# Kernel optimization log

Hardware: AMD Instinct MI355X
Metric: run time of the kernel (lower is better)

The kernel has to match this reference:

```python
import jax, jax.numpy as jnp
import numpy as np
from jax import lax

L1_PENALTY = 0.01
ALPHA = L1_PENALTY / (2.0 * 1024.0)  # matches self.l1_penalty = l1_penalty / (2*1024)
N_ITERS = 200      # fixed FISTA iteration budget (replaces sklearn CD to tol=1e-6)
POWER_ITERS = 30   # power iterations for Lipschitz constant


def setup_inputs() -> dict:
    key = jax.random.key(0)
    k1, k2 = jax.random.split(key)
    D = jax.random.normal(k1, (10000, 1024), dtype=jnp.float32)
    D = D / (jnp.linalg.norm(D, axis=1, keepdims=True) + 1e-12)  # unit-norm concept embeddings
    emb = jax.random.normal(k2, (128, 1024), dtype=jnp.float32)
    emb = emb / (jnp.linalg.norm(emb, axis=1, keepdims=True) + 1e-12)  # unit-norm CLIP embeddings
    return {"embedding": emb, "dictionary": D}


def _lipschitz(D):
    # Largest eigenvalue of (1/n) * X^T X where X = D.T (n = clip_dim = n_samples in sklearn's Lasso objective)
    n = jnp.asarray(D.shape[1], D.dtype)
    v = jnp.ones((D.shape[0],), D.dtype)

    def body(i, v):
        u = v @ D                 # [d]
        v = (u @ D.T) / n         # [K]
        return v / (jnp.linalg.norm(v) + 1e-12)

    v = lax.fori_loop(0, POWER_ITERS, body, v)
    u = v @ D
    return jnp.linalg.norm((u @ D.T) / n)


def _nn_lasso_fista(D, Y):
    # Batched nonnegative Lasso: min_w (1/(2n))||y - D^T w||^2 + alpha*||w||_1, w >= 0
    # Same objective sklearn.linear_model.Lasso(alpha, positive=True, fit_intercept=False) solves per sample.
    n = jnp.asarray(D.shape[1], D.dtype)
    L = _lipschitz(D)
    step = 1.0 / L
    thresh = step * jnp.asarray(ALPHA, D.dtype)
    B, K = Y.shape[0], D.shape[0]
    w0 = jnp.zeros((B, K), Y.dtype)

    def body(i, carry):
        w, z, t = carry
        grad = ((z @ D - Y) @ D.T) / n                 # [B,K] gradient of smooth part
        w_new = jnp.maximum(z - step * grad - thresh, 0.0)  # nonnegative soft-threshold prox
        t_new = 0.5 * (1.0 + jnp.sqrt(1.0 + 4.0 * t * t))
        z_new = w_new + ((t - 1.0) / t_new) * (w_new - w)
        return (w_new, z_new, t_new)

    w, _, _ = lax.fori_loop(0, N_ITERS, body, (w0, w0, jnp.asarray(1.0, Y.dtype)))
    return w


def reference(embedding, dictionary):
    # decompose: per-sample nonnegative Lasso weights, batched
    weights = _nn_lasso_fista(dictionary, embedding)          # [B, K]
    # recompose_vector: weights @ dictionary, then L2-normalize rows
    recon = weights @ dictionary                              # [B, d]
    recon = recon / (jnp.linalg.norm(recon, axis=1, keepdims=True) + 1e-12)
    # encode_vector: diag(recon @ embedding.T).sum() == sum_i <recon_i, emb_i>
    score = jnp.sum(recon * embedding)
    return (weights, score)
```

## Files before the change

### kernel.cpp

```cpp
#include <hip/hip_runtime.h>
#include <math.h>

#define N_ITERS 200
#define PRECISE_TAIL 16
#define FAST_ITERS (N_ITERS - PRECISE_TAIL)
#define B_DIM 128
#define K_DIM 10000
#define KP2 10240
#define KB  10048
#define D_DIM 1024
#define ALPHA_F 4.8828125e-6f
#define SPLITK 32
#define KSLICE 320
#define NSTEP1 10
#define LSCALE 2048.0f
#define INV_LSCALE 4.8828125e-4f

typedef unsigned short u16;
typedef __attribute__((ext_vector_type(8))) _Float16 f16x8;
typedef __attribute__((ext_vector_type(4))) float f32x4;
#define MFMA16 __builtin_amdgcn_mfma_f32_16x16x32_f16

__device__ __forceinline__ u16 f2h(float x) {
    _Float16 h = (_Float16)x;
    return __builtin_bit_cast(unsigned short, h);
}
__device__ __forceinline__ float h2f(u16 v) {
    _Float16 h = __builtin_bit_cast(_Float16, v);
    return (float)h;
}
__device__ __forceinline__ void split2h(float x, u16& h, u16& l) {
    u16 hh = f2h(x);
    h = hh;
    l = f2h((x - h2f(hh)) * LSCALE);
}
__device__ __forceinline__ int swz(int r) { return (r & 3) ^ ((r >> 2) & 1); }

__device__ __forceinline__ void gl2lds16(const u16* g, u16* l) {
    __builtin_amdgcn_global_load_lds(
        (const __attribute__((address_space(1))) unsigned int*)g,
        (__attribute__((address_space(3))) unsigned int*)l,
        16, 0, 0);
}

template<int TN, int KS, bool SP>
__device__ __forceinline__ void gcore(
        const u16* __restrict__ Ahg, const u16* __restrict__ Alg, size_t sA, int arow0,
        const u16* __restrict__ Bhg, const u16* __restrict__ Blg, size_t sB, int brow0,
        size_t k0, int nsteps, u16* lds, int t, f32x4 (*acc)[2]) {
    constexpr int MFRAG = (TN == 64) ? 4 : 2;
    constexpr int P = KS / 32;
    constexpr int NA = P * (SP ? 2 : 1);
    constexpr int AB0 = NA * 4096;
    constexpr int BPAN = TN * 32;
    constexpr int NBP = P * (SP ? 2 : 1);
    constexpr int BUFS = AB0 + NBP * BPAN;
    constexpr int LA = 2 * NA;
    constexpr int LB = (TN == 64) ? (SP ? 2 : 1) : 1;
    constexpr int NLD = LA + LB;
    int lane = t & 63, quad = lane >> 4, lr = lane & 15;
    int wv = t >> 6;
    int wm = (TN == 64) ? ((wv >> 1) * 64) : (wv * 32);
    int wn = (TN == 64) ? ((wv & 1) * 32) : 0;
    int r1 = t >> 2, qs = t & 3;
    int q1 = qs ^ swz(r1);
    const u16* pA[NA][2];
    #pragma unroll
    for (int pa = 0; pa < NA; ++pa) {
        const u16* base = (!SP || pa < P) ? Ahg : Alg;
        size_t kk = k0 + (size_t)(pa % P) * 32;
        pA[pa][0] = base + (size_t)(arow0 + r1) * sA + kk + q1 * 8;
        pA[pa][1] = base + (size_t)(arow0 + r1 + 64) * sA + kk + q1 * 8;
    }
    const u16* pB0;
    const u16* pB1 = nullptr;
    int bdst;
    if constexpr (TN == 64) {
        pB0 = Bhg + (size_t)(brow0 + r1) * sB + k0 + q1 * 8;
        if constexpr (SP) pB1 = Blg + (size_t)(brow0 + r1) * sB + k0 + q1 * 8;
        bdst = AB0 + t * 8;
    } else {
        int j = t >> 7;
        int rb = (t & 127) >> 2;
        int qb = qs ^ swz(rb);
        if constexpr (SP) {
            pB0 = (j ? Blg : Bhg) + (size_t)(brow0 + rb) * sB + k0 + qb * 8;
        } else {
            pB0 = Bhg + (size_t)(brow0 + rb) * sB + k0 + (size_t)j * 32 + qb * 8;
        }
        bdst = AB0 + j * BPAN + (t & 127) * 8;
    }
    int dA = t * 8;
    int offA[MFRAG], offB[2];
    #pragma unroll
    for (int mi = 0; mi < MFRAG; ++mi) { int rr = wm + mi * 16 + lr; offA[mi] = rr * 32 + ((quad ^ swz(rr)) * 8); }
    #pragma unroll
    for (int ni = 0; ni < 2; ++ni) { int rr = wn + ni * 16 + lr; offB[ni] = rr * 32 + ((quad ^ swz(rr)) * 8); }
    f32x4 accC[MFRAG][2];
    #pragma unroll
    for (int mi = 0; mi < MFRAG; ++mi)
        #pragma unroll
        for (int ni = 0; ni < 2; ++ni) { acc[mi][ni] = (f32x4){0.f,0.f,0.f,0.f}; accC[mi][ni] = (f32x4){0.f,0.f,0.f,0.f}; }

    auto stage = [&](u16* b, int c) {
        #pragma unroll
        for (int pa = 0; pa < NA; ++pa) {
            gl2lds16(pA[pa][0] + c, b + pa * 4096 + dA);
            gl2lds16(pA[pa][1] + c, b + pa * 4096 + 2048 + dA);
        }
        gl2lds16(pB0 + c, b + bdst);
        if constexpr (TN == 64 && SP) gl2lds16(pB1 + c, b + bdst + BPAN);
    };
    stage(lds, 0);
    if (nsteps > 1) stage(lds + BUFS, KS);

    for (int s = 0; s < nsteps; ++s) {
        if (s + 2 < nsteps) stage(lds + ((s + 2) % 3) * BUFS, (s + 2) * KS);
        if (s + 3 <= nsteps) {
            asm volatile("s_waitcnt vmcnt(%0)" : : "i"(2 * NLD) : "memory");
        } else if (s + 2 == nsteps) {
            asm volatile("s_waitcnt vmcnt(%0)" : : "i"(NLD) : "memory");
        } else {
            asm volatile("s_waitcnt vmcnt(0)" : : : "memory");
        }
        __builtin_amdgcn_s_barrier();
        u16* b = lds + (s % 3) * BUFS;
        #pragma unroll
        for (int p = 0; p < P; ++p) {
            f16x8 aH[MFRAG], bH[2];
            #pragma unroll
            for (int mi = 0; mi < MFRAG; ++mi) aH[mi] = *(const f16x8*)&b[p * 4096 + offA[mi]];
            #pragma unroll
            for (int ni = 0; ni < 2; ++ni) bH[ni] = *(const f16x8*)&b[AB0 + p * BPAN + offB[ni]];
            if constexpr (SP) {
                f16x8 aL[MFRAG], bL[2];
                #pragma unroll
                for (int mi = 0; mi < MFRAG; ++mi) aL[mi] = *(const f16x8*)&b[(P + p) * 4096 + offA[mi]];
                #pragma unroll
                for (int ni = 0; ni < 2; ++ni) bL[ni] = *(const f16x8*)&b[AB0 + (P + p) * BPAN + offB[ni]];
                #pragma unroll
                for (int mi = 0; mi < MFRAG; ++mi)
                    #pragma unroll
                    for (int ni = 0; ni < 2; ++ni) {
                        acc[mi][ni]  = MFMA16(aH[mi], bH[ni], acc[mi][ni], 0, 0, 0);
                        accC[mi][ni] = MFMA16(aL[mi], bH[ni], accC[mi][ni], 0, 0, 0);
                        accC[mi][ni] = MFMA16(aH[mi], bL[ni], accC[mi][ni], 0, 0, 0);
                    }
            } else {
                #pragma unroll
                for (int mi = 0; mi < MFRAG; ++mi)
                    #pragma unroll
                    for (int ni = 0; ni < 2; ++ni)
                        acc[mi][ni] = MFMA16(aH[mi], bH[ni], acc[mi][ni], 0, 0, 0);
            }
        }
        __builtin_amdgcn_s_barrier();
    }
    if constexpr (SP) {
        #pragma unroll
        for (int mi = 0; mi < MFRAG; ++mi)
            #pragma unroll
            for (int ni = 0; ni < 2; ++ni)
                #pragma unroll
                for (int r = 0; r < 4; ++r)
                    acc[mi][ni][r] += accC[mi][ni][r] * INV_LSCALE;
    }
}

__global__ __launch_bounds__(256) void k_init(float* __restrict__ out,
                                              u16* __restrict__ Zh, u16* __restrict__ Zl,
                                              u16* __restrict__ Wh,
                                              float* __restrict__ u0,
                                              float* __restrict__ scal) {
    int idx = blockIdx.x * 256 + threadIdx.x;
    int stride = gridDim.x * 256;
    for (int i = idx; i <= B_DIM * K_DIM; i += stride) out[i] = 0.0f;
    unsigned* zh = (unsigned*)Zh;
    unsigned* zl = (unsigned*)Zl;
    for (int i = idx; i < B_DIM * KP2 / 2; i += stride) { zh[i] = 0u; zl[i] = 0u; }
    unsigned* wh = (unsigned*)Wh;
    for (int i = idx; i < B_DIM * KB / 2; i += stride) wh[i] = 0u;
    for (int i = idx; i < 64; i += stride) scal[i] = 0.0f;
    for (int i = idx; i < D_DIM; i += stride) u0[i] = 0.0f;
}

__global__ __launch_bounds__(256) void k_convertD(const float* __restrict__ D,
                                                  u16* __restrict__ Dh,
                                                  u16* __restrict__ Dl,
                                                  u16* __restrict__ Dth,
                                                  u16* __restrict__ Dtl) {
    __shared__ u16 Th[32][33], Tl[32][33];
    int tx = threadIdx.x & 31, ty = threadIdx.x >> 5;
    int k0 = blockIdx.x * 32, d0 = blockIdx.y * 32;
    #pragma unroll
    for (int r = 0; r < 4; ++r) {
        int krow = k0 + ty + r * 8;
        float val = (krow < K_DIM) ? D[(size_t)krow * D_DIM + d0 + tx] : 0.0f;
        u16 h, l; split2h(val, h, l);
        if (krow < KB) {
            Dh[(size_t)krow * D_DIM + d0 + tx] = h;
            Dl[(size_t)krow * D_DIM + d0 + tx] = l;
        }
        Th[ty + r * 8][tx] = h;
        Tl[ty + r * 8][tx] = l;
    }
    __syncthreads();
    #pragma unroll
    for (int r = 0; r < 4; ++r) {
        int d = d0 + ty + r * 8;
        int k = k0 + tx;
        Dth[(size_t)d * KP2 + k] = Th[tx][ty + r * 8];
        Dtl[(size_t)d * KP2 + k] = Tl[tx][ty + r * 8];
    }
}

__global__ __launch_bounds__(256) void k_colsum(const float* __restrict__ D,
                                                float* __restrict__ u0) {
    int t = threadIdx.x;
    int kbase = blockIdx.x * 40;
    float a0 = 0.f, a1 = 0.f, a2 = 0.f, a3 = 0.f;
    for (int k = kbase; k < kbase + 40; ++k) {
        const float* row = D + (size_t)k * D_DIM;
        a0 += row[t];
        a1 += row[t + 256];
        a2 += row[t + 512];
        a3 += row[t + 768];
    }
    atomicAdd(&u0[t], a0);
    atomicAdd(&u0[t + 256], a1);
    atomicAdd(&u0[t + 512], a2);
    atomicAdd(&u0[t + 768], a3);
}

__global__ __launch_bounds__(256, 2) void k_gram(const u16* __restrict__ Dth,
                                                 const u16* __restrict__ Dtl,
                                                 float* __restrict__ G) {
    __shared__ __align__(16) u16 lds[3 * 12288];
    int t = threadIdx.x;
    int n0 = blockIdx.x * 64, m0 = blockIdx.y * 128;
    f32x4 acc[4][2];
    gcore<64, 32, true>(Dth, Dtl, KP2, m0, Dth, Dtl, KP2, n0, 0, 320, lds, t, acc);
    int lane = t & 63, quad = lane >> 4, lr = lane & 15;
    int wv = t >> 6;
    int wm = (wv >> 1) * 64, wn = (wv & 1) * 32;
    #pragma unroll
    for (int mi = 0; mi < 4; ++mi)
        #pragma unroll
        for (int ni = 0; ni < 2; ++ni) {
            int c = n0 + wn + ni * 16 + lr;
            #pragma unroll
            for (int r = 0; r < 4; ++r) {
                int row = m0 + wm + mi * 16 + quad * 4 + r;
                G[(size_t)row * D_DIM + c] = acc[mi][ni][r];
            }
        }
}

__global__ __launch_bounds__(256) void k_pstep(const float* __restrict__ G,
                                               const float* __restrict__ u0,
                                               const float* __restrict__ wvin,
                                               float* __restrict__ wvout,
                                               float* __restrict__ scal, int pw) {
    int t = threadIdx.x;
    int c = blockIdx.x * 4 + (t >> 6);
    int lane = t & 63;
    float rsX = (pw > 0) ? rsqrtf(scal[1 + pw]) : 1.0f;
    float a = 0.f;
    const float* Gr = G + (size_t)c * D_DIM;
    #pragma unroll
    for (int j = 0; j < 16; ++j) {
        int r = lane + j * 64;
        float ur = (pw == 0) ? u0[r] : wvin[r] * rsX;
        a = fmaf(ur, Gr[r], a);
    }
    #pragma unroll
    for (int o = 32; o > 0; o >>= 1) a += __shfl_down(a, o, 64);
    if (lane == 0) {
        float uc = (pw == 0) ? u0[c] : wvin[c] * rsX;
        wvout[c] = a;
        atomicAdd(&scal[2 + pw], a * uc);
    }
}

__global__ void k_Lfin(float* __restrict__ scal) {
    float stepv = 1024.0f / sqrtf(scal[2 + 30]);
    scal[0] = stepv;
    scal[1] = stepv * ALPHA_F;
}

__global__ __launch_bounds__(256, 2) void k_g1f(const u16* __restrict__ Zh,
                                                const u16* __restrict__ Dth,
                                                float* __restrict__ Up) {
    __shared__ __align__(16) u16 lds[3 * 6144];
    int t = threadIdx.x;
    int n0 = blockIdx.x * 64;
    int ks = blockIdx.y;
    f32x4 acc[4][2];
    gcore<64, 32, false>(Zh, nullptr, KP2, 0, Dth, nullptr, KP2, n0,
                         (size_t)ks * KSLICE, NSTEP1, lds, t, acc);
    int lane = t & 63, quad = lane >> 4, lr = lane & 15;
    int wv = t >> 6;
    int wm = (wv >> 1) * 64, wn = (wv & 1) * 32;
    float* o = Up + (size_t)ks * (B_DIM * D_DIM);
    #pragma unroll
    for (int mi = 0; mi < 4; ++mi)
        #pragma unroll
        for (int ni = 0; ni < 2; ++ni) {
            int d = n0 + wn + ni * 16 + lr;
            #pragma unroll
            for (int r = 0; r < 4; ++r) {
                int row = wm + mi * 16 + quad * 4 + r;
                o[(size_t)row * D_DIM + d] = acc[mi][ni][r];
            }
        }
}

__global__ __launch_bounds__(256, 2) void k_g1p(const u16* __restrict__ Zh,
                                                const u16* __restrict__ Zl,
                                                const u16* __restrict__ Dth,
                                                const u16* __restrict__ Dtl,
                                                float* __restrict__ Up) {
    __shared__ __align__(16) u16 lds[3 * 12288];
    int t = threadIdx.x;
    int n0 = blockIdx.x * 64;
    int ks = blockIdx.y;
    f32x4 acc[4][2];
    gcore<64, 32, true>(Zh, Zl, KP2, 0, Dth, Dtl, KP2, n0, (size_t)ks * KSLICE,
                        NSTEP1, lds, t, acc);
    int lane = t & 63, quad = lane >> 4, lr = lane & 15;
    int wv = t >> 6;
    int wm = (wv >> 1) * 64, wn = (wv & 1) * 32;
    float* o = Up + (size_t)ks * (B_DIM * D_DIM);
    #pragma unroll
    for (int mi = 0; mi < 4; ++mi)
        #pragma unroll
        for (int ni = 0; ni < 2; ++ni) {
            int d = n0 + wn + ni * 16 + lr;
            #pragma unroll
            for (int r = 0; r < 4; ++r) {
                int row = wm + mi * 16 + quad * 4 + r;
                o[(size_t)row * D_DIM + d] = acc[mi][ni][r];
            }
        }
}

__global__ __launch_bounds__(256) void k_redF(const float* __restrict__ Up,
                                              u16* __restrict__ Eh,
                                              const float* __restrict__ emb) {
    int base = (blockIdx.x * 256 + threadIdx.x) * 8;
    float4 s0 = {0, 0, 0, 0}, s1 = {0, 0, 0, 0};
    #pragma unroll
    for (int s = 0; s < SPLITK; ++s) {
        const float* p = Up + (size_t)s * (B_DIM * D_DIM) + base;
        float4 a = *(const float4*)p;
        float4 b = *(const float4*)(p + 4);
        s0.x += a.x; s0.y += a.y; s0.z += a.z; s0.w += a.w;
        s1.x += b.x; s1.y += b.y; s1.z += b.z; s1.w += b.w;
    }
    float4 e0 = *(const float4*)&emb[base];
    float4 e1 = *(const float4*)&emb[base + 4];
    float vbuf[8] = {s0.x - e0.x, s0.y - e0.y, s0.z - e0.z, s0.w - e0.w,
                     s1.x - e1.x, s1.y - e1.y, s1.z - e1.z, s1.w - e1.w};
    union { u16 us[8]; int4 v; } h;
    #pragma unroll
    for (int q = 0; q < 8; ++q) h.us[q] = f2h(vbuf[q]);
    *(int4*)&Eh[base] = h.v;
}

__global__ __launch_bounds__(256) void k_redP(const float* __restrict__ Up,
                                              u16* __restrict__ Eh,
                                              u16* __restrict__ El,
                                              const float* __restrict__ emb,
                                              int recon) {
    int base = (blockIdx.x * 256 + threadIdx.x) * 8;
    float4 s0 = {0, 0, 0, 0}, s1 = {0, 0, 0, 0};
    #pragma unroll
    for (int s = 0; s < SPLITK; ++s) {
        const float* p = Up + (size_t)s * (B_DIM * D_DIM) + base;
        float4 a = *(const float4*)p;
        float4 b = *(const float4*)(p + 4);
        s0.x += a.x; s0.y += a.y; s0.z += a.z; s0.w += a.w;
        s1.x += b.x; s1.y += b.y; s1.z += b.z; s1.w += b.w;
    }
    if (!recon) {
        float4 e0 = *(const float4*)&emb[base];
        float4 e1 = *(const float4*)&emb[base + 4];
        s0.x -= e0.x; s0.y -= e0.y; s0.z -= e0.z; s0.w -= e0.w;
        s1.x -= e1.x; s1.y -= e1.y; s1.z -= e1.z; s1.w -= e1.w;
    }
    float vbuf[8] = {s0.x, s0.y, s0.z, s0.w, s1.x, s1.y, s1.z, s1.w};
    union { u16 us[8]; int4 v; } h, l;
    #pragma unroll
    for (int q = 0; q < 8; ++q) split2h(vbuf[q], h.us[q], l.us[q]);
    *(int4*)&Eh[base] = h.v;
    *(int4*)&El[base] = l.v;
}

template<int EM>
__global__ __launch_bounds__(256, 2) void k_g2f(const u16* __restrict__ Eh,
                                                const u16* __restrict__ Dh,
                                                u16* __restrict__ Wh,
                                                float* __restrict__ W,
                                                u16* __restrict__ Zh,
                                                u16* __restrict__ Zl,
                                                const float* __restrict__ scal,
                                                float mom) {
    __shared__ __align__(16) u16 lds[3 * 10240];
    int t = threadIdx.x;
    int n0 = blockIdx.x * 32;
    f32x4 acc[2][2];
    gcore<32, 64, false>(Eh, nullptr, D_DIM, 0, Dh, nullptr, D_DIM, n0, 0,
                         16, lds, t, acc);
    int lane = t & 63, quad = lane >> 4, lr = lane & 15;
    int wm = (t >> 6) * 32;
    const float invN = 1.0f / 1024.0f;
    float stepv = scal[0], th = scal[1];
    #pragma unroll
    for (int mi = 0; mi < 2; ++mi)
        #pragma unroll
        for (int ni = 0; ni < 2; ++ni) {
            int k = n0 + ni * 16 + lr;
            #pragma unroll
            for (int r = 0; r < 4; ++r) {
                int i = wm + mi * 16 + quad * 4 + r;
                size_t iz = (size_t)i * KP2 + k;
                float g = acc[mi][ni][r] * invN;
                float z = h2f(Zh[iz]);
                float wold = h2f(Wh[(size_t)i * KB + k]);
                float wnew = fmaxf(z - stepv * g - th, 0.0f);
                float zn = wnew + mom * (wnew - wold);
                if constexpr (EM == 0) {
                    Wh[(size_t)i * KB + k] = f2h(wnew);
                    Zh[iz] = f2h(zn);
                } else {
                    if (k < K_DIM) W[(size_t)i * K_DIM + k] = wnew;
                    u16 h, l; split2h(zn, h, l);
                    Zh[iz] = h; Zl[iz] = l;
                }
            }
        }
}

__global__ __launch_bounds__(256, 2) void k_g2p(const u16* __restrict__ Eh,
                                                const u16* __restrict__ El,
                                                const u16* __restrict__ Dh,
                                                const u16* __restrict__ Dl,
                                                float* __restrict__ W,
                                                u16* __restrict__ Zh, u16* __restrict__ Zl,
                                                const float* __restrict__ scal,
                                                float mom, int writeW) {
    __shared__ __align__(16) u16 lds[3 * 10240];
    int t = threadIdx.x;
    int n0 = blockIdx.x * 32;
    f32x4 acc[2][2];
    gcore<32, 32, true>(Eh, El, D_DIM, 0, Dh, Dl, D_DIM, n0, 0, 32, lds, t, acc);
    int lane = t & 63, quad = lane >> 4, lr = lane & 15;
    int wm = (t >> 6) * 32;
    const float invN = 1.0f / 1024.0f;
    float stepv = scal[0], th = scal[1];
    #pragma unroll
    for (int mi = 0; mi < 2; ++mi)
        #pragma unroll
        for (int ni = 0; ni < 2; ++ni) {
            int k = n0 + ni * 16 + lr;
            #pragma unroll
            for (int r = 0; r < 4; ++r) {
                int i = wm + mi * 16 + quad * 4 + r;
                size_t iz = (size_t)i * KP2 + k;
                float g = acc[mi][ni][r] * invN;
                float z = h2f(Zh[iz]) + h2f(Zl[iz]) * INV_LSCALE;
                float wold = (k < K_DIM) ? W[(size_t)i * K_DIM + k] : 0.0f;
                float wnew = fmaxf(z - stepv * g - th, 0.0f);
                float zn = wnew + mom * (wnew - wold);
                if (k < K_DIM) W[(size_t)i * K_DIM + k] = wnew;
                u16 h, l;
                split2h(writeW ? wnew : zn, h, l);
                Zh[iz] = h; Zl[iz] = l;
            }
        }
}

__global__ __launch_bounds__(256) void k_score(const u16* __restrict__ Eh,
                                               const u16* __restrict__ El,
                                               const float* __restrict__ emb,
                                               float* __restrict__ score) {
    int wid = blockIdx.x * 4 + (threadIdx.x >> 6);
    int lane = threadIdx.x & 63;
    if (wid >= B_DIM) return;
    float rr = 0.f, re = 0.f;
    #pragma unroll
    for (int j = 0; j < D_DIM; j += 64) {
        int idx = wid * D_DIM + j + lane;
        float x = h2f(Eh[idx]) + h2f(El[idx]) * INV_LSCALE;
        rr = fmaf(x, x, rr);
        re = fmaf(x, emb[idx], re);
    }
    #pragma unroll
    for (int off = 32; off > 0; off >>= 1) {
        rr += __shfl_down(rr, off, 64);
        re += __shfl_down(re, off, 64);
    }
    if (lane == 0) atomicAdd(score, re / (sqrtf(rr) + 1e-12f));
}

extern "C" void kernel_launch(void* const* d_in, const int* in_sizes, int n_in,
                              void* d_out, int out_size, void* d_ws, size_t ws_size,
                              hipStream_t stream) {
    const float* emb = (const float*)d_in[0];
    const float* Dm  = (const float*)d_in[1];
    float* out = (float*)d_out;
    float* W = out;

    size_t off = 0;
    auto carve = [&](size_t bytes) -> void* {
        void* r = (char*)d_ws + off;
        off += (bytes + 255) & ~(size_t)255;
        return r;
    };
    float* G    = (float*)carve((size_t)D_DIM * D_DIM * 4);
    float* Up   = (float*)carve((size_t)SPLITK * B_DIM * D_DIM * 4);
    u16*   Zh   = (u16*)carve((size_t)B_DIM * KP2 * 2);
    u16*   Zl   = (u16*)carve((size_t)B_DIM * KP2 * 2);
    u16*   Wh   = (u16*)carve((size_t)B_DIM * KB * 2);
    u16*   Eh   = (u16*)carve((size_t)B_DIM * D_DIM * 2);
    u16*   El   = (u16*)carve((size_t)B_DIM * D_DIM * 2);
    float* u0   = (float*)carve(D_DIM * 4);
    float* wva  = (float*)carve(D_DIM * 4);
    float* wvb  = (float*)carve(D_DIM * 4);
    float* scal = (float*)carve(64 * 4);
    u16*   Dh   = (u16*)carve((size_t)KB * D_DIM * 2);
    u16*   Dl   = (u16*)carve((size_t)KB * D_DIM * 2);
    u16*   Dth  = (u16*)carve((size_t)D_DIM * KP2 * 2);
    u16*   Dtl  = (u16*)carve((size_t)D_DIM * KP2 * 2);

    k_init<<<512, 256, 0, stream>>>(out, Zh, Zl, Wh, u0, scal);
    k_convertD<<<dim3(320, 32), 256, 0, stream>>>(Dm, Dh, Dl, Dth, Dtl);
    k_colsum<<<250, 256, 0, stream>>>(Dm, u0);
    k_gram<<<dim3(16, 8), 256, 0, stream>>>(Dth, Dtl, G);

    for (int pw = 0; pw <= 30; ++pw) {
        float* win  = (pw & 1) ? wva : wvb;
        float* wout = (pw & 1) ? wvb : wva;
        k_pstep<<<256, 256, 0, stream>>>(G, u0, win, wout, scal, pw);
    }
    k_Lfin<<<1, 1, 0, stream>>>(scal);

    double t = 1.0;
    for (int it = 0; it < N_ITERS; ++it) {
        double tn = 0.5 * (1.0 + sqrt(1.0 + 4.0 * t * t));
        float mom = (float)((t - 1.0) / tn);
        t = tn;
        if (it < FAST_ITERS) {
            k_g1f<<<dim3(16, SPLITK), 256, 0, stream>>>(Zh, Dth, Up);
            k_redF<<<64, 256, 0, stream>>>(Up, Eh, emb);
            if (it == FAST_ITERS - 1)
                k_g2f<1><<<dim3(314, 1), 256, 0, stream>>>(Eh, Dh, Wh, W,
                                                           Zh, Zl, scal, mom);
            else
                k_g2f<0><<<dim3(314, 1), 256, 0, stream>>>(Eh, Dh, Wh, W,
                                                           Zh, Zl, scal, mom);
        } else {
            k_g1p<<<dim3(16, SPLITK), 256, 0, stream>>>(Zh, Zl, Dth, Dtl, Up);
            k_redP<<<64, 256, 0, stream>>>(Up, Eh, El, emb, 0);
            k_g2p<<<dim3(314, 1), 256, 0, stream>>>(Eh, El, Dh, Dl, W, Zh, Zl,
                                                    scal, mom,
                                                    (it == N_ITERS - 1) ? 1 : 0);
        }
    }

    k_g1p<<<dim3(16, SPLITK), 256, 0, stream>>>(Zh, Zl, Dth, Dtl, Up);
    k_redP<<<64, 256, 0, stream>>>(Up, Eh, El, emb, 1);
    k_score<<<32, 256, 0, stream>>>(Eh, El, emb, out + (size_t)B_DIM * K_DIM);
}
```

Baseline: 7.893 ms.

## Fuse split-K reduction into g1f via last-blocks ticket and deepen pipeline

Removes the separate k_redF launch in the fast iterations. k_g1f blocks now publish their partial products with cache-bypassing stores and take a ticket from a global counter. The last 64 blocks to arrive spin until every partial is written, then each reduces one slab and writes Eh. Separately, the gcore LDS pipeline depth becomes a template parameter, raised to 5 buffers for k_g1f. This saves a launch and its gap per iteration but adds spin-waiting, an atomic, and higher LDS use, which may lower occupancy.

New measurement: 15.01 ms. 1.9x slower.

```diff
diff --git a/kernel.cpp b/kernel.cpp
--- a/kernel.cpp
+++ b/kernel.cpp
@@ -15,6 +15,8 @@
 #define NSTEP1 10
 #define LSCALE 2048.0f
 #define INV_LSCALE 4.8828125e-4f
+#define G1_BLOCKS 512
+#define N_RED 64
 
 typedef unsigned short u16;
 typedef __attribute__((ext_vector_type(8))) _Float16 f16x8;
@@ -42,8 +44,11 @@
         (__attribute__((address_space(3))) unsigned int*)l,
         16, 0, 0);
 }
-
-template<int TN, int KS, bool SP>
+__device__ __forceinline__ void st_sc(float* p, float v) {
+    asm volatile("global_store_dword %0, %1, off sc0 sc1" : : "v"(p), "v"(v) : "memory");
+}
+
+template<int TN, int KS, bool SP, int NBUF>
 __device__ __forceinline__ void gcore(
         const u16* __restrict__ Ahg, const u16* __restrict__ Alg, size_t sA, int arow0,
         const u16* __restrict__ Bhg, const u16* __restrict__ Blg, size_t sB, int brow0,
@@ -111,20 +116,27 @@
         gl2lds16(pB0 + c, b + bdst);
         if constexpr (TN == 64 && SP) gl2lds16(pB1 + c, b + bdst + BPAN);
     };
-    stage(lds, 0);
-    if (nsteps > 1) stage(lds + BUFS, KS);
+    #pragma unroll
+    for (int i = 0; i < NBUF - 1; ++i)
+        if (i < nsteps) stage(lds + i * BUFS, i * KS);
 
     for (int s = 0; s < nsteps; ++s) {
-        if (s + 2 < nsteps) stage(lds + ((s + 2) % 3) * BUFS, (s + 2) * KS);
-        if (s + 3 <= nsteps) {
+        if (s + NBUF - 1 < nsteps)
+            stage(lds + ((s + NBUF - 1) % NBUF) * BUFS, (s + NBUF - 1) * KS);
+        int rem = nsteps - 1 - s;
+        if (rem >= NBUF - 1) {
+            asm volatile("s_waitcnt vmcnt(%0)" : : "i"((NBUF - 1) * NLD) : "memory");
+        } else if (NBUF >= 5 && rem == 3) {
+            asm volatile("s_waitcnt vmcnt(%0)" : : "i"(3 * NLD) : "memory");
+        } else if (NBUF >= 4 && rem == 2) {
             asm volatile("s_waitcnt vmcnt(%0)" : : "i"(2 * NLD) : "memory");
-        } else if (s + 2 == nsteps) {
+        } else if (rem == 1) {
             asm volatile("s_waitcnt vmcnt(%0)" : : "i"(NLD) : "memory");
         } else {
             asm volatile("s_waitcnt vmcnt(0)" : : : "memory");
         }
         __builtin_amdgcn_s_barrier();
-        u16* b = lds + (s % 3) * BUFS;
+        u16* b = lds + (s % NBUF) * BUFS;
         #pragma unroll
         for (int p = 0; p < P; ++p) {
             f16x8 aH[MFRAG], bH[2];
@@ -170,6 +182,7 @@
 __global__ __launch_bounds__(256) void k_init(float* __restrict__ out,
                                               u16* __restrict__ Zh, u16* __restrict__ Zl,
                                               u16* __restrict__ Wh,
+                                              int* __restrict__ sem,
                                               float* __restrict__ u0,
                                               float* __restrict__ scal) {
     int idx = blockIdx.x * 256 + threadIdx.x;
@@ -180,7 +193,7 @@
     for (int i = idx; i < B_DIM * KP2 / 2; i += stride) { zh[i] = 0u; zl[i] = 0u; }
     unsigned* wh = (unsigned*)Wh;
     for (int i = idx; i < B_DIM * KB / 2; i += stride) wh[i] = 0u;
-    for (int i = idx; i < 64; i += stride) scal[i] = 0.0f;
+    for (int i = idx; i < 64; i += stride) { scal[i] = 0.0f; sem[i] = 0; }
     for (int i = idx; i < D_DIM; i += stride) u0[i] = 0.0f;
 }
 
@@ -239,7 +252,7 @@
     int t = threadIdx.x;
     int n0 = blockIdx.x * 64, m0 = blockIdx.y * 128;
     f32x4 acc[4][2];
-    gcore<64, 32, true>(Dth, Dtl, KP2, m0, Dth, Dtl, KP2, n0, 0, 320, lds, t, acc);
+    gcore<64, 32, true, 3>(Dth, Dtl, KP2, m0, Dth, Dtl, KP2, n0, 0, 320, lds, t, acc);
     int lane = t & 63, quad = lane >> 4, lr = lane & 15;
     int wv = t >> 6;
     int wm = (wv >> 1) * 64, wn = (wv & 1) * 32;
@@ -290,14 +303,19 @@
 
 __global__ __launch_bounds__(256, 2) void k_g1f(const u16* __restrict__ Zh,
                                                 const u16* __restrict__ Dth,
-                                                float* __restrict__ Up) {
-    __shared__ __align__(16) u16 lds[3 * 6144];
+                                                float* __restrict__ Up,
+                                                u16* __restrict__ Eh,
+                                                const float* __restrict__ emb,
+                                                int* __restrict__ sem,
+                                                int tgt) {
+    __shared__ __align__(16) u16 lds[5 * 6144];
+    __shared__ int s_tick;
     int t = threadIdx.x;
     int n0 = blockIdx.x * 64;
     int ks = blockIdx.y;
     f32x4 acc[4][2];
-    gcore<64, 32, false>(Zh, nullptr, KP2, 0, Dth, nullptr, KP2, n0,
-                         (size_t)ks * KSLICE, NSTEP1, lds, t, acc);
+    gcore<64, 32, false, 5>(Zh, nullptr, KP2, 0, Dth, nullptr, KP2, n0,
+                            (size_t)ks * KSLICE, NSTEP1, lds, t, acc);
     int lane = t & 63, quad = lane >> 4, lr = lane & 15;
     int wv = t >> 6;
     int wm = (wv >> 1) * 64, wn = (wv & 1) * 32;
@@ -310,9 +328,65 @@
             #pragma unroll
             for (int r = 0; r < 4; ++r) {
                 int row = wm + mi * 16 + quad * 4 + r;
-                o[(size_t)row * D_DIM + d] = acc[mi][ni][r];
+                st_sc(&o[(size_t)row * D_DIM + d], acc[mi][ni][r]);
             }
         }
+    asm volatile("s_waitcnt vmcnt(0)" : : : "memory");
+    __threadfence();
+    __syncthreads();
+    if (t == 0)
+        s_tick = __hip_atomic_fetch_add(&sem[0], 1, __ATOMIC_ACQ_REL,
+                                        __HIP_MEMORY_SCOPE_AGENT);
+    __syncthreads();
+    int ticket = s_tick;
+    if (ticket < tgt - N_RED) return;
+    if (t == 0) {
+        while (__hip_atomic_load(&sem[0], __ATOMIC_ACQUIRE,
+                                 __HIP_MEMORY_SCOPE_AGENT) < tgt)
+            __builtin_amdgcn_s_sleep(2);
+    }
+    __syncthreads();
+    int slab = ticket - (tgt - N_RED);
+    int base = slab * (B_DIM * D_DIM / N_RED) + t * 8;
+    const float* up0 = Up + base;
+    f32x4 a0 = {0.f, 0.f, 0.f, 0.f}, a1 = {0.f, 0.f, 0.f, 0.f};
+    #pragma unroll
+    for (int g = 0; g < SPLITK / 4; ++g) {
+        const float* p0 = up0 + (size_t)(g * 4 + 0) * (B_DIM * D_DIM);
+        const float* p1 = p0 + 4;
+        const float* p2 = up0 + (size_t)(g * 4 + 1) * (B_DIM * D_DIM);
+        const float* p3 = p2 + 4;
+        const float* p4 = up0 + (size_t)(g * 4 + 2) * (B_DIM * D_DIM);
+        const float* p5 = p4 + 4;
+        const float* p6 = up0 + (size_t)(g * 4 + 3) * (B_DIM * D_DIM);
+        const float* p7 = p6 + 4;
+        f32x4 v0, v1, v2, v3, v4, v5, v6, v7;
+        asm volatile(
+            "global_load_dwordx4 %0, %8, off sc0 sc1\n\t"
+            "global_load_dwordx4 %1, %9, off sc0 sc1\n\t"
+            "global_load_dwordx4 %2, %10, off sc0 sc1\n\t"
+            "global_load_dwordx4 %3, %11, off sc0 sc1\n\t"
+            "global_load_dwordx4 %4, %12, off sc0 sc1\n\t"
+            "global_load_dwordx4 %5, %13, off sc0 sc1\n\t"
+            "global_load_dwordx4 %6, %14, off sc0 sc1\n\t"
+            "global_load_dwordx4 %7, %15, off sc0 sc1\n\t"
+            "s_waitcnt vmcnt(0)"
+            : "=&v"(v0), "=&v"(v1), "=&v"(v2), "=&v"(v3),
+              "=&v"(v4), "=&v"(v5), "=&v"(v6), "=&v"(v7)
+            : "v"(p0), "v"(p1), "v"(p2), "v"(p3),
+              "v"(p4), "v"(p5), "v"(p6), "v"(p7)
+            : "memory");
+        a0 += v0 + v2 + v4 + v6;
+        a1 += v1 + v3 + v5 + v7;
+    }
+    f32x4 e0 = *(const f32x4*)&emb[base];
+    f32x4 e1 = *(const f32x4*)&emb[base + 4];
+    a0 -= e0;
+    a1 -= e1;
+    union { u16 us[8]; int4 v; } h;
+    #pragma unroll
+    for (int q = 0; q < 4; ++q) { h.us[q] = f2h(a0[q]); h.us[4 + q] = f2h(a1[q]); }
+    *(int4*)&Eh[base] = h.v;
 }
 
 __global__ __launch_bounds__(256, 2) void k_g1p(const u16* __restrict__ Zh,
@@ -325,8 +399,8 @@
     int n0 = blockIdx.x * 64;
     int ks = blockIdx.y;
     f32x4 acc[4][2];
-    gcore<64, 32, true>(Zh, Zl, KP2, 0, Dth, Dtl, KP2, n0, (size_t)ks * KSLICE,
-                        NSTEP1, lds, t, acc);
+    gcore<64, 32, true, 3>(Zh, Zl, KP2, 0, Dth, Dtl, KP2, n0, (size_t)ks * KSLICE,
+                           NSTEP1, lds, t, acc);
     int lane = t & 63, quad = lane >> 4, lr = lane & 15;
     int wv = t >> 6;
     int wm = (wv >> 1) * 64, wn = (wv & 1) * 32;
@@ -342,29 +416,6 @@
                 o[(size_t)row * D_DIM + d] = acc[mi][ni][r];
             }
         }
-}
-
-__global__ __launch_bounds__(256) void k_redF(const float* __restrict__ Up,
-                                              u16* __restrict__ Eh,
-                                              const float* __restrict__ emb) {
-    int base = (blockIdx.x * 256 + threadIdx.x) * 8;
-    float4 s0 = {0, 0, 0, 0}, s1 = {0, 0, 0, 0};
-    #pragma unroll
-    for (int s = 0; s < SPLITK; ++s) {
-        const float* p = Up + (size_t)s * (B_DIM * D_DIM) + base;
-        float4 a = *(const float4*)p;
-        float4 b = *(const float4*)(p + 4);
-        s0.x += a.x; s0.y += a.y; s0.z += a.z; s0.w += a.w;
-        s1.x += b.x; s1.y += b.y; s1.z += b.z; s1.w += b.w;
-    }
-    float4 e0 = *(const float4*)&emb[base];
-    float4 e1 = *(const float4*)&emb[base + 4];
-    float vbuf[8] = {s0.x - e0.x, s0.y - e0.y, s0.z - e0.z, s0.w - e0.w,
-                     s1.x - e1.x, s1.y - e1.y, s1.z - e1.z, s1.w - e1.w};
-    union { u16 us[8]; int4 v; } h;
-    #pragma unroll
-    for (int q = 0; q < 8; ++q) h.us[q] = f2h(vbuf[q]);
-    *(int4*)&Eh[base] = h.v;
 }
 
 __global__ __launch_bounds__(256) void k_redP(const float* __restrict__ Up,
@@ -409,8 +460,8 @@
     int t = threadIdx.x;
     int n0 = blockIdx.x * 32;
     f32x4 acc[2][2];
-    gcore<32, 64, false>(Eh, nullptr, D_DIM, 0, Dh, nullptr, D_DIM, n0, 0,
-                         16, lds, t, acc);
+    gcore<32, 64, false, 3>(Eh, nullptr, D_DIM, 0, Dh, nullptr, D_DIM, n0, 0,
+                            16, lds, t, acc);
     int lane = t & 63, quad = lane >> 4, lr = lane & 15;
     int wm = (t >> 6) * 32;
     const float invN = 1.0f / 1024.0f;
@@ -453,7 +504,7 @@
     int t = threadIdx.x;
     int n0 = blockIdx.x * 32;
     f32x4 acc[2][2];
-    gcore<32, 32, true>(Eh, El, D_DIM, 0, Dh, Dl, D_DIM, n0, 0, 32, lds, t, acc);
+    gcore<32, 32, true, 3>(Eh, El, D_DIM, 0, Dh, Dl, D_DIM, n0, 0, 32, lds, t, acc);
     int lane = t & 63, quad = lane >> 4, lr = lane & 15;
     int wm = (t >> 6) * 32;
     const float invN = 1.0f / 1024.0f;
@@ -528,12 +579,13 @@
     float* wva  = (float*)carve(D_DIM * 4);
     float* wvb  = (float*)carve(D_DIM * 4);
     float* scal = (float*)carve(64 * 4);
+    int*   sem  = (int*)carve(64 * 4);
     u16*   Dh   = (u16*)carve((size_t)KB * D_DIM * 2);
     u16*   Dl   = (u16*)carve((size_t)KB * D_DIM * 2);
     u16*   Dth  = (u16*)carve((size_t)D_DIM * KP2 * 2);
     u16*   Dtl  = (u16*)carve((size_t)D_DIM * KP2 * 2);
 
-    k_init<<<512, 256, 0, stream>>>(out, Zh, Zl, Wh, u0, scal);
+    k_init<<<512, 256, 0, stream>>>(out, Zh, Zl, Wh, sem, u0, scal);
     k_convertD<<<dim3(320, 32), 256, 0, stream>>>(Dm, Dh, Dl, Dth, Dtl);
     k_colsum<<<250, 256, 0, stream>>>(Dm, u0);
     k_gram<<<dim3(16, 8), 256, 0, stream>>>(Dth, Dtl, G);
@@ -551,8 +603,9 @@
         float mom = (float)((t - 1.0) / tn);
         t = tn;
         if (it < FAST_ITERS) {
-            k_g1f<<<dim3(16, SPLITK), 256, 0, stream>>>(Zh, Dth, Up);
-            k_redF<<<64, 256, 0, stream>>>(Up, Eh, emb);
+            int tgt = G1_BLOCKS * (it + 1);
+            k_g1f<<<dim3(16, SPLITK), 256, 0, stream>>>(Zh, Dth, Up, Eh, emb,
+                                                        sem, tgt);
             if (it == FAST_ITERS - 1)
                 k_g2f<1><<<dim3(314, 1), 256, 0, stream>>>(Eh, Dh, Wh, W,
                                                            Zh, Zl, scal, mom);
```
